# Optimization experiments

Measured on AMD Instinct MI355X. Metric: run time of the kernel, lower is better.

## Reference

```python
import jax, jax.numpy as jnp
import numpy as np

N_NODES = 100000
N_EDGES = 1600000


def _spmm(row, col, val, x, n):
    # out[i] = sum_{e: row[e]==i} val[e] * x[col[e]]  (sparse adj @ dense x)
    return jax.ops.segment_sum(val[:, None] * x[col], row, num_segments=n)


def setup_inputs() -> dict:
    key = jax.random.key(0)
    ks = jax.random.split(key, 6)
    x = jax.random.normal(ks[0], (N_NODES, 128), dtype=jnp.float32)
    edge_row = jnp.sort(jax.random.randint(ks[1], (N_EDGES,), 0, N_NODES, dtype=jnp.int64))
    edge_col = jax.random.randint(ks[2], (N_EDGES,), 0, N_NODES, dtype=jnp.int64)
    # glorot-initialized linear layers (pyg Linear with weight_initializer='glorot')
    W0 = jax.random.normal(ks[3], (128, 128), dtype=jnp.float32) * np.sqrt(2.0 / (128 + 128))
    b0 = jnp.zeros((128,), dtype=jnp.float32)
    W1 = jax.random.normal(ks[4], (128, 64), dtype=jnp.float32) * np.sqrt(2.0 / (128 + 64))
    b1 = jnp.zeros((64,), dtype=jnp.float32)
    return {"x": x, "edge_row": edge_row, "edge_col": edge_col,
            "W0": W0, "b0": b0, "W1": W1, "b1": b1}


def reference(x, edge_row, edge_col, W0, b0, W1, b1):
    n = x.shape[0]
    # adj_norm: symmetric GCN normalization D^{-1/2} A D^{-1/2}
    ones = jnp.ones(edge_row.shape[0], dtype=x.dtype)
    deg = jax.ops.segment_sum(ones, edge_row, num_segments=n)
    dinv = jnp.where(deg > 0, jax.lax.rsqrt(jnp.maximum(deg, 1.0)), 0.0).astype(x.dtype)
    val = dinv[edge_row] * dinv[edge_col]
    # layer 0: linear -> SpMM -> relu (dropout is a no-op in inference/eval)
    h = x @ W0 + b0
    h = _spmm(edge_row, edge_col, val, h, n)
    h = jax.nn.relu(h)
    # layer 1: linear -> SpMM
    h = h @ W1 + b1
    h = _spmm(edge_row, edge_col, val, h, n)
    return jax.nn.log_softmax(h, axis=-1)
```

## Files before the change

### kernel.cpp

```cpp
#include <hip/hip_runtime.h>
#include <hip/hip_bf16.h>

#define NN 100000
#define NE 1600000

typedef __bf16 bf16x8 __attribute__((ext_vector_type(8)));
typedef float  f32x4  __attribute__((ext_vector_type(4)));

__global__ __launch_bounds__(256) void prep_kernel(const int* __restrict__ row,
                                                   int* __restrict__ row_ptr,
                                                   const float* __restrict__ W0,
                                                   const float* __restrict__ W1,
                                                   __hip_bfloat16* __restrict__ Wt0,
                                                   __hip_bfloat16* __restrict__ Wt1) {
    int b = blockIdx.x;
    if (b < NE / 256) {
        int e = b * 256 + threadIdx.x;
        int r  = row[e];
        int rp = (e == 0) ? -1 : row[e - 1];
        for (int i = rp + 1; i <= r; ++i) row_ptr[i] = e;
        if (e == NE - 1) {
            for (int i = r + 1; i <= NN; ++i) row_ptr[i] = NE;
        }
    } else {
        int idx = (b - NE / 256) * 256 + threadIdx.x;
        if (idx < 128 * 128) {
            int n = idx >> 7, k = idx & 127;
            Wt0[idx] = __float2bfloat16(W0[(size_t)k * 128 + n]);
        } else {
            int r2 = idx - 128 * 128;
            int n = r2 >> 7, k = r2 & 127;
            Wt1[r2] = __float2bfloat16(W1[(size_t)k * 64 + n]);
        }
    }
}

__device__ inline float deg_scale(const int* __restrict__ row_ptr, int i) {
    int dg = row_ptr[i + 1] - row_ptr[i];
    return (dg > 0) ? rsqrtf((float)dg) : 0.0f;
}

template <int NO, typename InT>
__global__ __launch_bounds__(512) void gemm_mfma(const InT* __restrict__ X,
                                                 const __hip_bfloat16* __restrict__ Wt,
                                                 const float* __restrict__ bias,
                                                 const int* __restrict__ row_ptr,
                                                 __hip_bfloat16* __restrict__ out, int M) {
    constexpr int NT = NO / 16;
    __shared__ unsigned short Ws[NO * 128];
    __shared__ unsigned short Cs[128 * 128];

    const int t = threadIdx.x;
    const int w = t >> 6, lane = t & 63;
    const int l15 = lane & 15, quad = lane >> 4;
    const int rbase = blockIdx.x * 128;

    for (int i = t; i < NO * 16; i += 512) {
        int n = i >> 4, g = i & 15;
        *(uint4*)&Ws[n * 128 + ((g ^ (n & 7)) << 3)] = ((const uint4*)Wt)[i];
    }
    __syncthreads();

    const int arow_g = rbase + w * 16 + l15;
    const int arow   = (arow_g < M) ? arow_g : (M - 1);

    bf16x8 af[4];
    if constexpr (sizeof(InT) == 4) {
        float4 lo[4], hi[4];
#pragma unroll
        for (int kc = 0; kc < 4; ++kc) {
            const float4* src = (const float4*)&X[(size_t)arow * 128 + kc * 32 + quad * 8];
            lo[kc] = src[0];
            hi[kc] = src[1];
        }
#pragma unroll
        for (int kc = 0; kc < 4; ++kc) {
            union { bf16x8 v; __hip_bfloat162 h[4]; } u;
            u.h[0] = __float22bfloat162_rn(make_float2(lo[kc].x, lo[kc].y));
            u.h[1] = __float22bfloat162_rn(make_float2(lo[kc].z, lo[kc].w));
            u.h[2] = __float22bfloat162_rn(make_float2(hi[kc].x, hi[kc].y));
            u.h[3] = __float22bfloat162_rn(make_float2(hi[kc].z, hi[kc].w));
            af[kc] = u.v;
        }
    } else {
        union { bf16x8 v; uint4 q; } u[4];
#pragma unroll
        for (int kc = 0; kc < 4; ++kc)
            u[kc].q = *(const uint4*)&X[(size_t)arow * 128 + kc * 32 + quad * 8];
#pragma unroll
        for (int kc = 0; kc < 4; ++kc) af[kc] = u[kc].v;
    }

    f32x4 acc[NT];
#pragma unroll
    for (int nt = 0; nt < NT; ++nt) {
        float bv = bias[nt * 16 + l15];
        acc[nt][0] = bv; acc[nt][1] = bv; acc[nt][2] = bv; acc[nt][3] = bv;
    }

#pragma unroll
    for (int kc = 0; kc < 4; ++kc) {
#pragma unroll
        for (int nt = 0; nt < NT; ++nt) {
            int brow = nt * 16 + l15;
            bf16x8 bfr = *(const bf16x8*)&Ws[brow * 128 + (((kc * 4 + quad) ^ (brow & 7)) << 3)];
            acc[nt] = __builtin_amdgcn_mfma_f32_16x16x32_bf16(af[kc], bfr, acc[nt], 0, 0, 0);
        }
    }

    __hip_bfloat16* Cp = (__hip_bfloat16*)Cs;
#pragma unroll
    for (int r4 = 0; r4 < 4; ++r4) {
        int lrow = w * 16 + quad * 4 + r4;
        int grow = rbase + lrow;
        float sc = (grow < M) ? deg_scale(row_ptr, grow) : 0.f;
#pragma unroll
        for (int nt = 0; nt < NT; ++nt) {
            int ct = nt * 16 + l15;
            Cp[lrow * 128 + ((((ct >> 3) ^ (lrow & 7)) << 3)) + (ct & 7)] =
                __float2bfloat16(acc[nt][r4] * sc);
        }
    }
    constexpr int RJ  = NO / 8;
    constexpr int CNT = (16 * RJ) / 64;
#pragma unroll
    for (int k = 0; k < CNT; ++k) {
        int idx = k * 64 + lane;
        int lr16 = idx / RJ, j = idx % RJ;
        int lrow = w * 16 + lr16;
        int grow = rbase + lrow;
        if (grow < M) {
            uint4 v = *(const uint4*)&Cp[lrow * 128 + ((j ^ (lrow & 7)) << 3)];
            *(uint4*)&out[(size_t)grow * NO + (j << 3)] = v;
        }
    }
}

__global__ __launch_bounds__(512) void spmm_relu_gemm1(const int* __restrict__ row_ptr,
                                                       const int* __restrict__ col,
                                                       const unsigned int* __restrict__ H,
                                                       const __hip_bfloat16* __restrict__ Wt1,
                                                       const float* __restrict__ b1,
                                                       __hip_bfloat16* __restrict__ out) {
    __shared__ unsigned short As[32 * 128];
    __shared__ unsigned short Ws[64 * 128];

    const int t = threadIdx.x;
    const int w = t >> 6, lane = t & 63;
    const int l15 = lane & 15, quad = lane >> 4;
    const int rbase = blockIdx.x * 32;

    for (int i = t; i < 64 * 16; i += 512) {
        int n = i >> 4, g = i & 15;
        *(uint4*)&Ws[n * 128 + ((g ^ (n & 7)) << 3)] = ((const uint4*)Wt1)[i];
    }

    const int gsw = ((lane >> 2) << 3) + ((lane & 3) << 1);
#pragma unroll 1
    for (int rr = 0; rr < 4; ++rr) {
        const int il = w * 4 + rr;
        const int i  = rbase + il;
        const int e0 = __builtin_amdgcn_readfirstlane(row_ptr[i]);
        const int e1 = __builtin_amdgcn_readfirstlane(row_ptr[i + 1]);
        const int dg = e1 - e0;
        const float di = (dg > 0) ? rsqrtf((float)dg) : 0.0f;
        float accx = 0.f, accy = 0.f;
        int e = e0;
        for (; e + 16 <= e1; e += 16) {
            unsigned int u[16];
#pragma unroll
            for (int j = 0; j < 16; ++j) {
                int c = __builtin_amdgcn_readfirstlane(col[e + j]);
                u[j] = H[(size_t)c * 64 + lane];
            }
#pragma unroll
            for (int j = 0; j < 16; ++j) {
                accx += __uint_as_float(u[j] << 16);
                accy += __uint_as_float(u[j] & 0xffff0000u);
            }
        }
        for (; e + 8 <= e1; e += 8) {
            unsigned int u[8];
#pragma unroll
            for (int j = 0; j < 8; ++j) {
                int c = __builtin_amdgcn_readfirstlane(col[e + j]);
                u[j] = H[(size_t)c * 64 + lane];
            }
#pragma unroll
            for (int j = 0; j < 8; ++j) {
                accx += __uint_as_float(u[j] << 16);
                accy += __uint_as_float(u[j] & 0xffff0000u);
            }
        }
        for (; e < e1; ++e) {
            int c = __builtin_amdgcn_readfirstlane(col[e]);
            unsigned int u = H[(size_t)c * 64 + lane];
            accx += __uint_as_float(u << 16);
            accy += __uint_as_float(u & 0xffff0000u);
        }
        accx = fmaxf(accx * di, 0.f);
        accy = fmaxf(accy * di, 0.f);
        union { __hip_bfloat162 h; unsigned int uu; } p;
        p.h = __float22bfloat162_rn(make_float2(accx, accy));
        *(unsigned int*)&As[il * 128 + ((((lane >> 2) ^ (il & 7)) << 3) + ((lane & 3) << 1))] = p.uu;
    }
    __syncthreads();

    const int rb = (w & 1) * 16;
    const int cb = (w >> 1) * 16;
    const int arow_l = rb + l15;
    const int asw = arow_l & 7;

    f32x4 acc;
    {
        float bv = b1[cb + l15];
        acc[0] = bv; acc[1] = bv; acc[2] = bv; acc[3] = bv;
    }
#pragma unroll
    for (int kc = 0; kc < 4; ++kc) {
        bf16x8 af = *(const bf16x8*)&As[arow_l * 128 + (((kc * 4 + quad) ^ asw) << 3)];
        int brow = cb + l15;
        bf16x8 bfr = *(const bf16x8*)&Ws[brow * 128 + (((kc * 4 + quad) ^ (brow & 7)) << 3)];
        acc = __builtin_amdgcn_mfma_f32_16x16x32_bf16(af, bfr, acc, 0, 0, 0);
    }

#pragma unroll
    for (int r4 = 0; r4 < 4; ++r4) {
        int grow = rbase + rb + quad * 4 + r4;
        float sc = deg_scale(row_ptr, grow);
        out[(size_t)grow * 64 + cb + l15] = __float2bfloat16(acc[r4] * sc);
    }
}

__global__ __launch_bounds__(256) void spmm_logsoftmax_64(const int* __restrict__ row_ptr,
                                                          const int* __restrict__ col,
                                                          const unsigned short* __restrict__ H,
                                                          float* __restrict__ out, int N) {
    const int lane = threadIdx.x & 63;
    int i = __builtin_amdgcn_readfirstlane(blockIdx.x * 4 + (threadIdx.x >> 6));
    if (i >= N) return;
    const int e0 = __builtin_amdgcn_readfirstlane(row_ptr[i]);
    const int e1 = __builtin_amdgcn_readfirstlane(row_ptr[i + 1]);
    const int dg = e1 - e0;
    const float di = (dg > 0) ? rsqrtf((float)dg) : 0.0f;
    float acc = 0.f;
    int e = e0;
    for (; e + 16 <= e1; e += 16) {
        unsigned short u[16];
#pragma unroll
        for (int j = 0; j < 16; ++j) {
            int c = __builtin_amdgcn_readfirstlane(col[e + j]);
            u[j] = H[(size_t)c * 64 + lane];
        }
#pragma unroll
        for (int j = 0; j < 16; ++j)
            acc += __uint_as_float((unsigned int)u[j] << 16);
    }
    for (; e + 8 <= e1; e += 8) {
        unsigned short u[8];
#pragma unroll
        for (int j = 0; j < 8; ++j) {
            int c = __builtin_amdgcn_readfirstlane(col[e + j]);
            u[j] = H[(size_t)c * 64 + lane];
        }
#pragma unroll
        for (int j = 0; j < 8; ++j)
            acc += __uint_as_float((unsigned int)u[j] << 16);
    }
    for (; e < e1; ++e) {
        int c = __builtin_amdgcn_readfirstlane(col[e]);
        acc += __uint_as_float((unsigned int)H[(size_t)c * 64 + lane] << 16);
    }
    acc *= di;
    float m = acc;
#pragma unroll
    for (int off = 32; off > 0; off >>= 1)
        m = fmaxf(m, __shfl_xor(m, off, 64));
    float ex = __expf(acc - m);
    float s = ex;
#pragma unroll
    for (int off = 32; off > 0; off >>= 1)
        s += __shfl_xor(s, off, 64);
    out[(size_t)i * 64 + lane] = acc - m - __logf(s);
}

extern "C" void kernel_launch(void* const* d_in, const int* in_sizes, int n_in,
                              void* d_out, int out_size, void* d_ws, size_t ws_size,
                              hipStream_t stream) {
    const float* x    = (const float*)d_in[0];
    const int*   erow = (const int*)d_in[1];
    const int*   ecol = (const int*)d_in[2];
    const float* W0   = (const float*)d_in[3];
    const float* b0   = (const float*)d_in[4];
    const float* W1   = (const float*)d_in[5];
    const float* b1   = (const float*)d_in[6];
    float* out = (float*)d_out;

    char* ws = (char*)d_ws;
    int*             row_ptr = (int*)ws;
    __hip_bfloat16*  h0b     = (__hip_bfloat16*)(ws + (1u << 20));
    __hip_bfloat16*  h2b     = (__hip_bfloat16*)(ws + 27000000u);
    __hip_bfloat16*  Wt0     = (__hip_bfloat16*)(ws + 41000000u);
    __hip_bfloat16*  Wt1     = (__hip_bfloat16*)(ws + 41100000u);

    prep_kernel<<<NE / 256 + 96, 256, 0, stream>>>(erow, row_ptr, W0, W1, Wt0, Wt1);
    gemm_mfma<128, float><<<(NN + 127) / 128, 512, 0, stream>>>(x, Wt0, b0, row_ptr, h0b, NN);
    spmm_relu_gemm1<<<NN / 32, 512, 0, stream>>>(row_ptr, ecol,
                                                 (const unsigned int*)h0b, Wt1, b1, h2b);
    spmm_logsoftmax_64<<<(NN + 3) / 4, 256, 0, stream>>>(row_ptr, ecol,
                                                         (const unsigned short*)h2b, out, NN);
}
```

Measured before the change: 237.7 us.

## Gather several edges per wavefront with 16-byte loads in both SpMM kernels

Both SpMM kernels now split each wavefront into lane groups, where each group gathers a different edge's row using 16-byte loads. Partial sums are then combined with cross-lane shuffles, replacing the old one-edge-per-wave pattern of 4- or 2-byte loads. The log-softmax kernel writes its output with float4 stores from one lane group, and the GEMM kernel reuses a single shared buffer for weights and output staging, adding a barrier to cut LDS use. The aim is fewer memory instructions and more edges in flight, at the cost of extra shuffle reductions and wasted lanes on the masked tail for low-degree rows.

```diff
diff --git a/kernel.cpp b/kernel.cpp
--- a/kernel.cpp
+++ b/kernel.cpp
@@ -6,6 +6,19 @@
 
 typedef __bf16 bf16x8 __attribute__((ext_vector_type(8)));
 typedef float  f32x4  __attribute__((ext_vector_type(4)));
+
+__device__ inline int rfl(int x) { return __builtin_amdgcn_readfirstlane(x); }
+
+__device__ inline void acc2(float& a, float& b, unsigned int u) {
+    a += __uint_as_float(u << 16);
+    b += __uint_as_float(u & 0xffff0000u);
+}
+
+__device__ inline unsigned int pack_bf2(float x, float y) {
+    union { __hip_bfloat162 h; unsigned int u; } p;
+    p.h = __float22bfloat162_rn(make_float2(x, y));
+    return p.u;
+}
 
 __global__ __launch_bounds__(256) void prep_kernel(const int* __restrict__ row,
                                                    int* __restrict__ row_ptr,
@@ -47,8 +60,7 @@
                                                  const int* __restrict__ row_ptr,
                                                  __hip_bfloat16* __restrict__ out, int M) {
     constexpr int NT = NO / 16;
-    __shared__ unsigned short Ws[NO * 128];
-    __shared__ unsigned short Cs[128 * 128];
+    __shared__ unsigned short SH[128 * 128];
 
     const int t = threadIdx.x;
     const int w = t >> 6, lane = t & 63;
@@ -57,7 +69,7 @@
 
     for (int i = t; i < NO * 16; i += 512) {
         int n = i >> 4, g = i & 15;
-        *(uint4*)&Ws[n * 128 + ((g ^ (n & 7)) << 3)] = ((const uint4*)Wt)[i];
+        *(uint4*)&SH[n * 128 + ((g ^ (n & 7)) << 3)] = ((const uint4*)Wt)[i];
     }
     __syncthreads();
 
@@ -103,12 +115,13 @@
 #pragma unroll
         for (int nt = 0; nt < NT; ++nt) {
             int brow = nt * 16 + l15;
-            bf16x8 bfr = *(const bf16x8*)&Ws[brow * 128 + (((kc * 4 + quad) ^ (brow & 7)) << 3)];
+            bf16x8 bfr = *(const bf16x8*)&SH[brow * 128 + (((kc * 4 + quad) ^ (brow & 7)) << 3)];
             acc[nt] = __builtin_amdgcn_mfma_f32_16x16x32_bf16(af[kc], bfr, acc[nt], 0, 0, 0);
         }
     }
-
-    __hip_bfloat16* Cp = (__hip_bfloat16*)Cs;
+    __syncthreads();
+
+    __hip_bfloat16* Cp = (__hip_bfloat16*)SH;
 #pragma unroll
     for (int r4 = 0; r4 < 4; ++r4) {
         int lrow = w * 16 + quad * 4 + r4;
@@ -138,7 +151,7 @@
 
 __global__ __launch_bounds__(512) void spmm_relu_gemm1(const int* __restrict__ row_ptr,
                                                        const int* __restrict__ col,
-                                                       const unsigned int* __restrict__ H,
+                                                       const uint4* __restrict__ H4,
                                                        const __hip_bfloat16* __restrict__ Wt1,
                                                        const float* __restrict__ b1,
                                                        __hip_bfloat16* __restrict__ out) {
@@ -149,60 +162,73 @@
     const int w = t >> 6, lane = t & 63;
     const int l15 = lane & 15, quad = lane >> 4;
     const int rbase = blockIdx.x * 32;
+    const int p = lane >> 4;
+    const int q = lane & 15;
 
     for (int i = t; i < 64 * 16; i += 512) {
         int n = i >> 4, g = i & 15;
         *(uint4*)&Ws[n * 128 + ((g ^ (n & 7)) << 3)] = ((const uint4*)Wt1)[i];
     }
 
-    const int gsw = ((lane >> 2) << 3) + ((lane & 3) << 1);
 #pragma unroll 1
     for (int rr = 0; rr < 4; ++rr) {
         const int il = w * 4 + rr;
         const int i  = rbase + il;
-        const int e0 = __builtin_amdgcn_readfirstlane(row_ptr[i]);
-        const int e1 = __builtin_amdgcn_readfirstlane(row_ptr[i + 1]);
+        const int e0 = rfl(row_ptr[i]);
+        const int e1 = rfl(row_ptr[i + 1]);
         const int dg = e1 - e0;
         const float di = (dg > 0) ? rsqrtf((float)dg) : 0.0f;
-        float accx = 0.f, accy = 0.f;
+        float a0 = 0.f, a1 = 0.f, a2 = 0.f, a3 = 0.f,
+              a4 = 0.f, a5 = 0.f, a6 = 0.f, a7 = 0.f;
         int e = e0;
         for (; e + 16 <= e1; e += 16) {
-            unsigned int u[16];
-#pragma unroll
-            for (int j = 0; j < 16; ++j) {
-                int c = __builtin_amdgcn_readfirstlane(col[e + j]);
-                u[j] = H[(size_t)c * 64 + lane];
+            uint4 v[4];
+#pragma unroll
+            for (int g2 = 0; g2 < 4; ++g2) {
+                int eb = e + g2 * 4;
+                int s0 = rfl(col[eb]), s1 = rfl(col[eb + 1]);
+                int s2 = rfl(col[eb + 2]), s3 = rfl(col[eb + 3]);
+                int c01 = (p & 1) ? s1 : s0;
+                int c23 = (p & 1) ? s3 : s2;
+                int c   = (p & 2) ? c23 : c01;
+                v[g2] = H4[(size_t)c * 16 + q];
             }
 #pragma unroll
-            for (int j = 0; j < 16; ++j) {
-                accx += __uint_as_float(u[j] << 16);
-                accy += __uint_as_float(u[j] & 0xffff0000u);
+            for (int g2 = 0; g2 < 4; ++g2) {
+                acc2(a0, a1, v[g2].x); acc2(a2, a3, v[g2].y);
+                acc2(a4, a5, v[g2].z); acc2(a6, a7, v[g2].w);
             }
         }
-        for (; e + 8 <= e1; e += 8) {
-            unsigned int u[8];
-#pragma unroll
-            for (int j = 0; j < 8; ++j) {
-                int c = __builtin_amdgcn_readfirstlane(col[e + j]);
-                u[j] = H[(size_t)c * 64 + lane];
-            }
-#pragma unroll
-            for (int j = 0; j < 8; ++j) {
-                accx += __uint_as_float(u[j] << 16);
-                accy += __uint_as_float(u[j] & 0xffff0000u);
-            }
-        }
-        for (; e < e1; ++e) {
-            int c = __builtin_amdgcn_readfirstlane(col[e]);
-            unsigned int u = H[(size_t)c * 64 + lane];
-            accx += __uint_as_float(u << 16);
-            accy += __uint_as_float(u & 0xffff0000u);
-        }
-        accx = fmaxf(accx * di, 0.f);
-        accy = fmaxf(accy * di, 0.f);
-        union { __hip_bfloat162 h; unsigned int uu; } p;
-        p.h = __float22bfloat162_rn(make_float2(accx, accy));
-        *(unsigned int*)&As[il * 128 + ((((lane >> 2) ^ (il & 7)) << 3) + ((lane & 3) << 1))] = p.uu;
+        for (; e < e1; e += 4) {
+            int em = e1 - 1;
+            int j1 = (e + 1 > em) ? em : e + 1;
+            int j2 = (e + 2 > em) ? em : e + 2;
+            int j3 = (e + 3 > em) ? em : e + 3;
+            int s0 = rfl(col[e]),  s1 = rfl(col[j1]);
+            int s2 = rfl(col[j2]), s3 = rfl(col[j3]);
+            int c01 = (p & 1) ? s1 : s0;
+            int c23 = (p & 1) ? s3 : s2;
+            int c   = (p & 2) ? c23 : c01;
+            uint4 v = H4[(size_t)c * 16 + q];
+            if (e + p >= e1) { v.x = 0u; v.y = 0u; v.z = 0u; v.w = 0u; }
+            acc2(a0, a1, v.x); acc2(a2, a3, v.y);
+            acc2(a4, a5, v.z); acc2(a6, a7, v.w);
+        }
+#pragma unroll
+        for (int off = 16; off < 64; off <<= 1) {
+            a0 += __shfl_xor(a0, off, 64); a1 += __shfl_xor(a1, off, 64);
+            a2 += __shfl_xor(a2, off, 64); a3 += __shfl_xor(a3, off, 64);
+            a4 += __shfl_xor(a4, off, 64); a5 += __shfl_xor(a5, off, 64);
+            a6 += __shfl_xor(a6, off, 64); a7 += __shfl_xor(a7, off, 64);
+        }
+        if (p == 0) {
+            uint4 pk;
+            pk.x = pack_bf2(fmaxf(a0 * di, 0.f), fmaxf(a1 * di, 0.f));
+            pk.y = pack_bf2(fmaxf(a2 * di, 0.f), fmaxf(a3 * di, 0.f));
+            pk.z = pack_bf2(fmaxf(a4 * di, 0.f), fmaxf(a5 * di, 0.f));
+            pk.w = pack_bf2(fmaxf(a6 * di, 0.f), fmaxf(a7 * di, 0.f));
+            *(uint4*)&As[il * 128 + ((q ^ (il & 7)) << 3)] = pk;
+        }
     }
     __syncthreads();
 
@@ -234,54 +260,78 @@
 
 __global__ __launch_bounds__(256) void spmm_logsoftmax_64(const int* __restrict__ row_ptr,
                                                           const int* __restrict__ col,
-                                                          const unsigned short* __restrict__ H,
+                                                          const uint4* __restrict__ H4,
                                                           float* __restrict__ out, int N) {
     const int lane = threadIdx.x & 63;
-    int i = __builtin_amdgcn_readfirstlane(blockIdx.x * 4 + (threadIdx.x >> 6));
+    const int p = lane >> 3;
+    const int q = lane & 7;
+    int i = rfl(blockIdx.x * 4 + (threadIdx.x >> 6));
     if (i >= N) return;
-    const int e0 = __builtin_amdgcn_readfirstlane(row_ptr[i]);
-    const int e1 = __builtin_amdgcn_readfirstlane(row_ptr[i + 1]);
+    const int e0 = rfl(row_ptr[i]);
+    const int e1 = rfl(row_ptr[i + 1]);
     const int dg = e1 - e0;
     const float di = (dg > 0) ? rsqrtf((float)dg) : 0.0f;
-    float acc = 0.f;
+    float a0 = 0.f, a1 = 0.f, a2 = 0.f, a3 = 0.f,
+          a4 = 0.f, a5 = 0.f, a6 = 0.f, a7 = 0.f;
     int e = e0;
-    for (; e + 16 <= e1; e += 16) {
-        unsigned short u[16];
-#pragma unroll
-        for (int j = 0; j < 16; ++j) {
-            int c = __builtin_amdgcn_readfirstlane(col[e + j]);
-            u[j] = H[(size_t)c * 64 + lane];
-        }
-#pragma unroll
-        for (int j = 0; j < 16; ++j)
-            acc += __uint_as_float((unsigned int)u[j] << 16);
-    }
     for (; e + 8 <= e1; e += 8) {
-        unsigned short u[8];
-#pragma unroll
-        for (int j = 0; j < 8; ++j) {
-            int c = __builtin_amdgcn_readfirstlane(col[e + j]);
-            u[j] = H[(size_t)c * 64 + lane];
-        }
-#pragma unroll
-        for (int j = 0; j < 8; ++j)
-            acc += __uint_as_float((unsigned int)u[j] << 16);
-    }
-    for (; e < e1; ++e) {
-        int c = __builtin_amdgcn_readfirstlane(col[e]);
-        acc += __uint_as_float((unsigned int)H[(size_t)c * 64 + lane] << 16);
-    }
-    acc *= di;
-    float m = acc;
-#pragma unroll
-    for (int off = 32; off > 0; off >>= 1)
+        int s0 = rfl(col[e + 0]), s1 = rfl(col[e + 1]);
+        int s2 = rfl(col[e + 2]), s3 = rfl(col[e + 3]);
+        int s4 = rfl(col[e + 4]), s5 = rfl(col[e + 5]);
+        int s6 = rfl(col[e + 6]), s7 = rfl(col[e + 7]);
+        int b0 = (p & 1) ? s1 : s0, b1_ = (p & 1) ? s3 : s2;
+        int b2 = (p & 1) ? s5 : s4, b3_ = (p & 1) ? s7 : s6;
+        int c0 = (p & 2) ? b1_ : b0, c1 = (p & 2) ? b3_ : b2;
+        int c  = (p & 4) ? c1 : c0;
+        uint4 v = H4[(size_t)c * 8 + q];
+        acc2(a0, a1, v.x); acc2(a2, a3, v.y);
+        acc2(a4, a5, v.z); acc2(a6, a7, v.w);
+    }
+    for (; e < e1; e += 8) {
+        int em = e1 - 1;
+        int k1 = (e + 1 > em) ? em : e + 1, k2 = (e + 2 > em) ? em : e + 2;
+        int k3 = (e + 3 > em) ? em : e + 3, k4 = (e + 4 > em) ? em : e + 4;
+        int k5 = (e + 5 > em) ? em : e + 5, k6 = (e + 6 > em) ? em : e + 6;
+        int k7 = (e + 7 > em) ? em : e + 7;
+        int s0 = rfl(col[e]),  s1 = rfl(col[k1]);
+        int s2 = rfl(col[k2]), s3 = rfl(col[k3]);
+        int s4 = rfl(col[k4]), s5 = rfl(col[k5]);
+        int s6 = rfl(col[k6]), s7 = rfl(col[k7]);
+        int b0 = (p & 1) ? s1 : s0, b1_ = (p & 1) ? s3 : s2;
+        int b2 = (p & 1) ? s5 : s4, b3_ = (p & 1) ? s7 : s6;
+        int c0 = (p & 2) ? b1_ : b0, c1 = (p & 2) ? b3_ : b2;
+        int c  = (p & 4) ? c1 : c0;
+        uint4 v = H4[(size_t)c * 8 + q];
+        if (e + p >= e1) { v.x = 0u; v.y = 0u; v.z = 0u; v.w = 0u; }
+        acc2(a0, a1, v.x); acc2(a2, a3, v.y);
+        acc2(a4, a5, v.z); acc2(a6, a7, v.w);
+    }
+#pragma unroll
+    for (int off = 8; off < 64; off <<= 1) {
+        a0 += __shfl_xor(a0, off, 64); a1 += __shfl_xor(a1, off, 64);
+        a2 += __shfl_xor(a2, off, 64); a3 += __shfl_xor(a3, off, 64);
+        a4 += __shfl_xor(a4, off, 64); a5 += __shfl_xor(a5, off, 64);
+        a6 += __shfl_xor(a6, off, 64); a7 += __shfl_xor(a7, off, 64);
+    }
+    a0 *= di; a1 *= di; a2 *= di; a3 *= di;
+    a4 *= di; a5 *= di; a6 *= di; a7 *= di;
+    float m = fmaxf(fmaxf(fmaxf(a0, a1), fmaxf(a2, a3)),
+                    fmaxf(fmaxf(a4, a5), fmaxf(a6, a7)));
+#pragma unroll
+    for (int off = 1; off < 8; off <<= 1)
         m = fmaxf(m, __shfl_xor(m, off, 64));
-    float ex = __expf(acc - m);
-    float s = ex;
-#pragma unroll
-    for (int off = 32; off > 0; off >>= 1)
+    float s = __expf(a0 - m) + __expf(a1 - m) + __expf(a2 - m) + __expf(a3 - m)
+            + __expf(a4 - m) + __expf(a5 - m) + __expf(a6 - m) + __expf(a7 - m);
+#pragma unroll
+    for (int off = 1; off < 8; off <<= 1)
         s += __shfl_xor(s, off, 64);
-    out[(size_t)i * 64 + lane] = acc - m - __logf(s);
+    float ls = __logf(s);
+    if (p == 0) {
+        float4 o0 = make_float4(a0 - m - ls, a1 - m - ls, a2 - m - ls, a3 - m - ls);
+        float4 o1 = make_float4(a4 - m - ls, a5 - m - ls, a6 - m - ls, a7 - m - ls);
+        *(float4*)&out[(size_t)i * 64 + q * 8]     = o0;
+        *(float4*)&out[(size_t)i * 64 + q * 8 + 4] = o1;
+    }
 }
 
 extern "C" void kernel_launch(void* const* d_in, const int* in_sizes, int n_in,
@@ -306,7 +356,7 @@
     prep_kernel<<<NE / 256 + 96, 256, 0, stream>>>(erow, row_ptr, W0, W1, Wt0, Wt1);
     gemm_mfma<128, float><<<(NN + 127) / 128, 512, 0, stream>>>(x, Wt0, b0, row_ptr, h0b, NN);
     spmm_relu_gemm1<<<NN / 32, 512, 0, stream>>>(row_ptr, ecol,
-                                                 (const unsigned int*)h0b, Wt1, b1, h2b);
+                                                 (const uint4*)h0b, Wt1, b1, h2b);
     spmm_logsoftmax_64<<<(NN + 3) / 4, 256, 0, stream>>>(row_ptr, ecol,
-                                                         (const unsigned short*)h2b, out, NN);
-}
+                                                         (const uint4*)h2b, out, NN);
+}
```

Measured after the change: 228.1 us. 4.0% less time.
